# Kernel tuning notes

Hardware: AMD Instinct MI355X
Metric: run time of the kernel (lower is better)

Reference implementation:

```python
import jax, jax.numpy as jnp
import numpy as np

T_MAX = 20  # max_seq_length


def setup_inputs() -> dict:
    key = jax.random.key(0)
    ks = jax.random.split(key, 24)
    B, H, A, V, Tc = 64, 512, 512, 50257, 19
    s = 0.02
    inp = {}
    inp["features"] = jax.random.normal(ks[0], (B, H), jnp.float32)
    inp["captions"] = jax.random.randint(ks[1], (B, Tc), 0, V)
    lens = jax.random.randint(ks[2], (B, 1), 1, T_MAX + 1)
    inp["lengths"] = -jnp.sort(-lens, axis=0)  # descending so sort_ind is identity
    inp["embed_table"] = jax.random.uniform(ks[3], (V, H), jnp.float32, -0.1, 0.1)
    # LSTM cell (PyTorch layout): input = [emb; attended] -> 2H
    inp["W_ih"] = jax.random.normal(ks[4], (4 * H, 2 * H), jnp.float32) * s
    inp["W_hh"] = jax.random.normal(ks[5], (4 * H, H), jnp.float32) * s
    inp["b_ih"] = jnp.zeros((4 * H,), jnp.float32)
    inp["b_hh"] = jnp.zeros((4 * H,), jnp.float32)
    # attention
    inp["W_enc"] = jax.random.normal(ks[6], (H, A), jnp.float32) * s
    inp["b_enc"] = jnp.zeros((A,), jnp.float32)
    inp["W_dec"] = jax.random.normal(ks[7], (H, A), jnp.float32) * s
    inp["b_dec"] = jnp.zeros((A,), jnp.float32)
    inp["W_full"] = jax.random.normal(ks[8], (A, 1), jnp.float32) * s
    inp["b_full"] = jnp.zeros((1,), jnp.float32)
    # init_h / init_c / f_beta / fc
    inp["W_hinit"] = jax.random.normal(ks[9], (H, H), jnp.float32) * s
    inp["b_hinit"] = jnp.zeros((H,), jnp.float32)
    inp["W_cinit"] = jax.random.normal(ks[10], (H, H), jnp.float32) * s
    inp["b_cinit"] = jnp.zeros((H,), jnp.float32)
    inp["W_beta"] = jax.random.normal(ks[11], (H, H), jnp.float32) * s
    inp["b_beta"] = jnp.zeros((H,), jnp.float32)
    inp["W_fc"] = jax.random.uniform(ks[12], (H, V), jnp.float32, -0.1, 0.1)
    inp["b_fc"] = jnp.zeros((V,), jnp.float32)
    return inp


def _decode(features, embed_table, W_ih, W_hh, b_ih, b_hh, W_enc, b_enc,
            W_dec, b_dec, W_full, b_full, W_hinit, b_hinit, W_cinit, b_cinit,
            W_beta, b_beta, W_fc, b_fc, captions, lengths):
    B, H = features.shape
    emb = embed_table[captions]                               # (B, T-1, H)
    embeddings = jnp.concatenate([features[:, None, :], emb], axis=1)  # (B, T, H)
    encoder_out = features[:, None, :]                        # (B, 1, H) num_pixels=1
    mean_enc = encoder_out.mean(axis=1)
    h0 = mean_enc @ W_hinit + b_hinit
    c0 = mean_enc @ W_cinit + b_cinit
    att1 = encoder_out @ W_enc + b_enc                        # (B, 1, A), time-invariant
    lens = lengths[:, 0]

    def step(carry, xs):
        h, c = carry
        emb_t, t = xs
        # attention
        att2 = h @ W_dec + b_dec                              # (B, A)
        e = jax.nn.relu(att1 + att2[:, None, :]) @ W_full + b_full  # (B, 1, 1)
        alpha = jax.nn.softmax(e[..., 0], axis=1)             # (B, 1)
        awe = (encoder_out * alpha[..., None]).sum(axis=1)    # (B, H)
        gate = jax.nn.sigmoid(h @ W_beta + b_beta)
        awe = gate * awe
        # LSTM cell (PyTorch gate order i, f, g, o)
        x = jnp.concatenate([emb_t, awe], axis=1)             # (B, 2H)
        gates = x @ W_ih.T + b_ih + h @ W_hh.T + b_hh
        i, f, g, o = jnp.split(gates, 4, axis=1)
        c_new = jax.nn.sigmoid(f) * c + jax.nn.sigmoid(i) * jnp.tanh(g)
        h_new = jax.nn.sigmoid(o) * jnp.tanh(c_new)
        preds = h_new @ W_fc + b_fc                           # (B, V)
        mask = (t < lens)[:, None]
        h = jnp.where(mask, h_new, h)
        c = jnp.where(mask, c_new, c)
        out_t = jnp.where(mask, preds, jnp.zeros_like(preds))
        return (h, c), out_t

    xs = (embeddings.transpose(1, 0, 2), jnp.arange(T_MAX))
    _, outs = jax.lax.scan(step, (h0, c0), xs)                # (T, B, V)
    return outs.transpose(1, 0, 2)                            # (B, T, V)


def reference(features, captions, lengths, embed_table, W_ih, W_hh, b_ih, b_hh,
              W_enc, b_enc, W_dec, b_dec, W_full, b_full, W_hinit, b_hinit,
              W_cinit, b_cinit, W_beta, b_beta, W_fc, b_fc):
    return _decode(features, embed_table, W_ih, W_hh, b_ih, b_hh, W_enc, b_enc,
                   W_dec, b_dec, W_full, b_full, W_hinit, b_hinit, W_cinit,
                   b_cinit, W_beta, b_beta, W_fc, b_fc, captions, lengths)
```

## Files before the change

### kernel.cpp

```cpp
#include <hip/hip_runtime.h>
#include <hip/hip_bf16.h>


#define VV 50257
#define VP 50304
#define TT 20
#define NWRK 32
#define NTILES 6288

typedef __attribute__((ext_vector_type(4))) float f32x4;
typedef __attribute__((ext_vector_type(8))) short bf16x8;

#define MFMA(a,b,c) __builtin_amdgcn_mfma_f32_16x16x32_bf16((a),(b),(c),0,0,0)

__device__ __forceinline__ unsigned short f2bf(float f){
  union { float f; unsigned int u; } v; v.f = f;
  unsigned int u = v.u;
  return (unsigned short)((u + 0x7FFFu + ((u >> 16) & 1u)) >> 16);
}
__device__ __forceinline__ float sigf(float x){ return 1.f/(1.f + expf(-x)); }

__device__ __forceinline__ void gload_lds16(const unsigned short* g, unsigned short* l){
  __builtin_amdgcn_global_load_lds(
      (const __attribute__((address_space(1))) unsigned int*)g,
      (__attribute__((address_space(3))) unsigned int*)l, 16, 0, 0);
}

__device__ __forceinline__ void co_load16(bf16x8* d, const unsigned short* p){
  asm volatile("global_load_dwordx4 %0, %1, off sc0 sc1" : "=v"(*d) : "v"(p));
}
__device__ __forceinline__ void co_store2(unsigned short* p, unsigned short v){
  asm volatile("global_store_short %0, %1, off sc0 sc1" :: "v"(p), "v"(v) : "memory");
}
__device__ __forceinline__ unsigned int co_load_u32(const unsigned int* p){
  unsigned int r;
  asm volatile("global_load_dword %0, %1, off sc0 sc1\n\ts_waitcnt vmcnt(0)"
               : "=v"(r) : "v"(p) : "memory");
  return r;
}
__device__ __forceinline__ void co_store_u32(unsigned int* p, unsigned int v){
  asm volatile("global_store_dword %0, %1, off sc0 sc1" :: "v"(p), "v"(v) : "memory");
}

__device__ __forceinline__ void gbar(unsigned int* flags, int widx, unsigned target){
  asm volatile("s_waitcnt vmcnt(0)" ::: "memory");
  __syncthreads();
  if(threadIdx.x == 0){
    co_store_u32(flags + widx, target);
  }
  if(threadIdx.x < 64){
    const unsigned int* p = flags + (threadIdx.x & 31);
    for(;;){
      unsigned v = co_load_u32(p);
      if(__all((int)(v >= target))) break;
      __builtin_amdgcn_s_sleep(1);
    }
  }
  __syncthreads();
}

__global__ __launch_bounds__(256) void prep(const float* __restrict__ Wih,
    const float* __restrict__ Whh, unsigned short* __restrict__ Wcomb,
    unsigned short* __restrict__ We,
    const float* __restrict__ Wbeta, unsigned short* __restrict__ Wbt,
    const float* __restrict__ feat, const float* __restrict__ emb,
    const int* __restrict__ cap, unsigned short* __restrict__ EmbMat,
    const float* __restrict__ Whi, const float* __restrict__ bhi,
    const float* __restrict__ Wci, const float* __restrict__ bci,
    unsigned short* __restrict__ xbuf, float* __restrict__ cbuf){
  __shared__ float tile[64][65];
  const int blk = blockIdx.x, tid = threadIdx.x;
  if(blk < 2048){
    int j = blk;
    for(int q=0;q<4;q++){ int k = tid + 256*q;
      float v = (k < 512) ? Whh[j*512 + k] : Wih[j*1024 + k];
      Wcomb[(size_t)j*1024 + k] = f2bf(v); }
    for(int q=0;q<2;q++){ int k = tid + 256*q;
      We[(size_t)j*512 + k] = f2bf(Wih[j*1024 + k]); }
  } else if(blk < 2112){
    int tb = blk - 2048;
    int c0 = (tb & 7)*64, r0 = (tb >> 3)*64;
    int tx = tid & 63, ty = tid >> 6;
    for(int i=0;i<16;i++){
      int r = ty + i*4;
      tile[r][tx] = Wbeta[(size_t)(r0+r)*512 + c0 + tx];
    }
    __syncthreads();
    for(int i=0;i<16;i++){
      int cl = ty + i*4;
      Wbt[(size_t)(c0+cl)*512 + r0 + tx] = f2bf(tile[tx][cl]);
    }
  } else if(blk < 3392){
    int m = blk - 2112; int t = m >> 6, b = m & 63;
    const float* src = (t == 0) ? (feat + b*512) : (emb + (size_t)cap[b*19 + (t-1)]*512);
    for(int q=0;q<2;q++){ int k = tid + 256*q;
      EmbMat[(size_t)m*512 + k] = f2bf(src[k]); }
  } else {
    int b = blk - 3392;
    float ah0 = bhi[tid], ah1 = bhi[tid+256];
    float ac0 = bci[tid], ac1 = bci[tid+256];
    for(int k=0;k<512;k++){
      float f = feat[b*512 + k];
      ah0 += f * Whi[k*512 + tid];     ah1 += f * Whi[k*512 + tid + 256];
      ac0 += f * Wci[k*512 + tid];     ac1 += f * Wci[k*512 + tid + 256];
    }
    xbuf[b*512 + tid] = f2bf(ah0);  xbuf[b*512 + tid + 256] = f2bf(ah1);
    cbuf[b*512 + tid] = ac0;        cbuf[b*512 + tid + 256] = ac1;
  }
}

__global__ __launch_bounds__(256) void gemmE(const unsigned short* __restrict__ Abf,
    const unsigned short* __restrict__ Bbf, const float* __restrict__ bias1,
    const float* __restrict__ bias2, float* __restrict__ Cout, int MT){
  __shared__ __align__(16) unsigned short As[128*64];
  __shared__ __align__(16) unsigned short Bs[128*64];
  const int nwg = gridDim.x;
  const int id = blockIdx.x;
  const int q = nwg >> 3, rr = nwg & 7;
  const int xcd = id & 7, pos = id >> 3;
  const int work = (xcd < rr) ? (xcd*(q+1) + pos) : (rr*(q+1) + (xcd-rr)*q + pos);
  const int m0 = (work % MT) * 128;
  const int n0 = (work / MT) * 128;
  const int tid = threadIdx.x, lane = tid & 63, w = tid >> 6;
  const int wr = w >> 1, wc = w & 1;
  const int lrow = lane >> 3, lcol = (lane & 7) * 8;
  const int l15 = lane & 15, lhi = lane >> 4;

  f32x4 acc[4][4];
#pragma unroll
  for(int i=0;i<4;i++)
#pragma unroll
    for(int j=0;j<4;j++) acc[i][j] = f32x4{0.f,0.f,0.f,0.f};

  for(int k0=0;k0<512;k0+=64){
    __syncthreads();
#pragma unroll
    for(int i=0;i<4;i++){
      int c = w*4 + i;
      int row = c*8 + lrow;
      gload_lds16(Abf + (size_t)(m0+row)*512 + k0 + lcol, As + c*512);
      gload_lds16(Bbf + (size_t)(n0+row)*512 + k0 + lcol, Bs + c*512);
    }
    asm volatile("s_waitcnt vmcnt(0)" ::: "memory");
    __syncthreads();
#pragma unroll
    for(int kk=0;kk<64;kk+=32){
      bf16x8 af[4], bfv[4];
#pragma unroll
      for(int mf=0;mf<4;mf++)
        af[mf] = *(const bf16x8*)(As + (wr*64 + mf*16 + l15)*64 + kk + lhi*8);
#pragma unroll
      for(int nf=0;nf<4;nf++)
        bfv[nf] = *(const bf16x8*)(Bs + (wc*64 + nf*16 + l15)*64 + kk + lhi*8);
#pragma unroll
      for(int mf=0;mf<4;mf++)
#pragma unroll
        for(int nf=0;nf<4;nf++)
          acc[mf][nf] = MFMA(af[mf], bfv[nf], acc[mf][nf]);
    }
  }
#pragma unroll
  for(int mf=0;mf<4;mf++)
#pragma unroll
    for(int nf=0;nf<4;nf++){
      int n = n0 + wc*64 + nf*16 + l15;
#pragma unroll
      for(int r=0;r<4;r++){
        int m = m0 + wr*64 + mf*16 + lhi*4 + r;
        int gate = n >> 9, col = n & 511;
        Cout[((size_t)m*512 + col)*4 + gate] = acc[mf][nf][r] + bias1[n] + bias2[n];
      }
    }
}

__global__ __launch_bounds__(256) void recur(
    const unsigned short* __restrict__ Wcomb,
    const unsigned short* __restrict__ Wbt,
    const float* __restrict__ bbeta,
    const float* __restrict__ feat,
    const float* __restrict__ E4,
    const float* __restrict__ c0,
    const int* __restrict__ lens,
    unsigned short* xbuf,
    unsigned short* awbuf,
    unsigned short* __restrict__ hs,
    unsigned int* ctrs,
    const float* __restrict__ Wfc, unsigned short* __restrict__ Wfct){
  extern __shared__ char LDS[];
  char* WCb = LDS;
  char* WBb = LDS + 131072;
  int* lsh = (int*)LDS;
  const int tid = threadIdx.x;

  if(tid == 0){
    unsigned xcc = 99;
    asm volatile("s_getreg_b32 %0, hwreg(HW_REG_XCC_ID)" : "=s"(xcc));
    unsigned my = 0xffffffffu;
    if(xcc == 0) my = atomicAdd(&ctrs[0], 1u);
    lsh[0] = (my < NWRK) ? 1 : 0;
    lsh[1] = (int)my;
  }
  __syncthreads();
  const int iswork = lsh[0];
  const int widx = lsh[1];
  __syncthreads();

  if(!iswork){
    float (*tile)[65] = (float(*)[65])LDS;
    int tx = tid & 63, ty = tid >> 6;
    for(;;){
      __syncthreads();
      if(tid == 0) lsh[0] = (int)atomicAdd(&ctrs[16], 1u);
      __syncthreads();
      int tb = lsh[0];
      __syncthreads();
      if(tb >= NTILES) return;
      int c0t = (tb % 786)*64, r0 = (tb / 786)*64;
      for(int i=0;i<16;i++){
        int r = ty + i*4; int sc = c0t + tx;
        tile[r][tx] = (sc < VV) ? Wfc[(size_t)(r0+r)*VV + sc] : 0.f;
      }
      __syncthreads();
      for(int i=0;i<16;i++){
        int cl = ty + i*4;
        Wfct[(size_t)(c0t+cl)*512 + r0 + tx] = f2bf(tile[tx][cl]);
      }
    }
  }

  const int lane = tid & 63, w = tid >> 6;
  const int l15 = lane & 15, lhi = lane >> 4;
  const int jj0 = widx * 16;
  const int jj = jj0 + l15;
  const int arow = w*16 + l15;
  unsigned int* flags = &ctrs[32];

  for(int cid = tid; cid < 8192; cid += 256){
    int gr = cid >> 7, cc = cid & 127;
    size_t g = (size_t)(gr >> 4)*512 + jj0 + (gr & 15);
    bf16x8 v = *(const bf16x8*)(Wcomb + g*1024 + cc*8);
    *(bf16x8*)(WCb + gr*2048 + ((cc*16) ^ ((gr & 7) << 4))) = v;
  }
  for(int cid = tid; cid < 1024; cid += 256){
    int r = cid >> 6, cc = cid & 63;
    bf16x8 v = *(const bf16x8*)(Wbt + (size_t)(jj0 + r)*512 + cc*8);
    *(bf16x8*)(WBb + r*1024 + ((cc*16) ^ ((r & 7) << 4))) = v;
  }

  float c_reg[4], fe[4]; int ln[4]; unsigned short hold[4];
#pragma unroll
  for(int r=0;r<4;r++){
    int b = w*16 + lhi*4 + r;
    c_reg[r] = c0[b*512 + jj];
    fe[r]    = feat[b*512 + jj];
    ln[r]    = lens[b];
    hold[r]  = xbuf[b*512 + jj];
  }
  const float bb = bbeta[jj];
  const unsigned short* pAx = xbuf  + (size_t)arow*512 + lhi*8;
  const unsigned short* pAw = awbuf + (size_t)arow*512 + lhi*8;
  __syncthreads();

  for(int t=0;t<TT;t++){
    f32x4 e4v[4];
#pragma unroll
    for(int r=0;r<4;r++){
      int b = w*16 + lhi*4 + r;
      e4v[r] = *(const f32x4*)(E4 + (((size_t)(t*64 + b))*512 + jj)*4);
    }
    bf16x8 a[16];
#pragma unroll
    for(int i=0;i<16;i++) co_load16(&a[i], pAx + i*32);
    asm volatile("s_waitcnt vmcnt(0)" ::: "memory");
    __builtin_amdgcn_sched_barrier(0);

    f32x4 acca = f32x4{0.f,0.f,0.f,0.f};
    f32x4 accg[4];
#pragma unroll
    for(int i=0;i<4;i++) accg[i] = f32x4{0.f,0.f,0.f,0.f};
#pragma unroll
    for(int i=0;i<16;i++){
      int kb2 = i*64 + lhi*16;
      bf16x8 wb = *(const bf16x8*)(WBb + l15*1024 + (kb2 ^ ((l15 & 7) << 4)));
      acca = MFMA(a[i], wb, acca);
#pragma unroll
      for(int nf=0; nf<4; nf++){
        int gr = nf*16 + l15;
        bf16x8 wg = *(const bf16x8*)(WCb + gr*2048 + (kb2 ^ ((gr & 7) << 4)));
        accg[nf] = MFMA(a[i], wg, accg[nf]);
      }
    }
#pragma unroll
    for(int r=0;r<4;r++){
      int b = w*16 + lhi*4 + r;
      float g = sigf(acca[r] + bb);
      co_store2(awbuf + b*512 + jj, f2bf(g * fe[r]));
    }
    gbar(flags, widx, (unsigned)(2*t+1));

#pragma unroll
    for(int i=0;i<16;i++) co_load16(&a[i], pAw + i*32);
    asm volatile("s_waitcnt vmcnt(0)" ::: "memory");
    __builtin_amdgcn_sched_barrier(0);
#pragma unroll
    for(int i=0;i<16;i++){
      int kb2 = 1024 + i*64 + lhi*16;
#pragma unroll
      for(int nf=0; nf<4; nf++){
        int gr = nf*16 + l15;
        bf16x8 wg = *(const bf16x8*)(WCb + gr*2048 + (kb2 ^ ((gr & 7) << 4)));
        accg[nf] = MFMA(a[i], wg, accg[nf]);
      }
    }

#pragma unroll
    for(int r=0;r<4;r++){
      int b = w*16 + lhi*4 + r;
      float iv = sigf(accg[0][r] + e4v[r][0]);
      float fv = sigf(accg[1][r] + e4v[r][1]);
      float gv = tanhf(accg[2][r] + e4v[r][2]);
      float ov = sigf(accg[3][r] + e4v[r][3]);
      float cn = fv*c_reg[r] + iv*gv;
      float hn = ov * tanhf(cn);
      bool valid = t < ln[r];
      if(valid) c_reg[r] = cn;
      unsigned short hb = valid ? f2bf(hn) : hold[r];
      hold[r] = hb;
      hs[((size_t)(t*64 + b))*512 + jj] = hb;
      co_store2(xbuf + b*512 + jj, hb);
    }
    if(t < TT-1) gbar(flags, widx, (unsigned)(2*t+2));
  }
}

__global__ __launch_bounds__(256) void outgemm(
    const unsigned short* __restrict__ hs,
    const unsigned short* __restrict__ Wfct,
    const float* __restrict__ bfc, const int* __restrict__ lens,
    float* __restrict__ out){
  extern __shared__ char LDS[];
  unsigned short* Bs = (unsigned short*)LDS;
  float* et = (float*)(LDS + 131072);
  const int tid = threadIdx.x, lane = tid & 63, w = tid >> 6;
  const int l15 = lane & 15, lhi = lane >> 4;
  const int n0 = blockIdx.x * 128;

#pragma unroll
  for(int i=0;i<32;i++){
    int cid = tid + 256*i;
    int row = cid >> 6, cc = cid & 63;
    bf16x8 v = *(const bf16x8*)(Wfct + (size_t)(n0 + row)*512 + cc*8);
    *(bf16x8*)((char*)Bs + row*1024 + ((cc*16) ^ ((row & 7) << 4))) = v;
  }
  float bias[8]; int lnv[4];
#pragma unroll
  for(int nf=0;nf<8;nf++){
    int n = n0 + nf*16 + l15;
    bias[nf] = (n < VV) ? bfc[n] : 0.f;
  }
#pragma unroll
  for(int r=0;r<4;r++) lnv[r] = lens[w*16 + lhi*4 + r];
  __syncthreads();
  const bool edge = (n0 + 128 > VV);

  for(int t=0;t<TT;t++){
    bf16x8 af[16];
    const unsigned short* pA = hs + (size_t)(t*64 + w*16 + l15)*512 + lhi*8;
#pragma unroll
    for(int i=0;i<16;i++) af[i] = *(const bf16x8*)(pA + i*32);
    f32x4 acc[8];
#pragma unroll
    for(int nf=0;nf<8;nf++) acc[nf] = f32x4{0.f,0.f,0.f,0.f};
#pragma unroll
    for(int i=0;i<16;i++){
      int kb2 = i*64 + lhi*16;
#pragma unroll
      for(int nf=0;nf<8;nf++){
        int gr = nf*16 + l15;
        bf16x8 bv = *(const bf16x8*)((char*)Bs + gr*1024 + (kb2 ^ ((gr & 7) << 4)));
        acc[nf] = MFMA(af[i], bv, acc[nf]);
      }
    }
    for(int h=0; h<2; h++){
      __syncthreads();
      if((w >> 1) == h){
#pragma unroll
        for(int nf=0;nf<8;nf++){
#pragma unroll
          for(int r=0;r<4;r++){
            bool valid = t < lnv[r];
            float v = valid ? (acc[nf][r] + bias[nf]) : 0.f;
            et[((w & 1)*16 + lhi*4 + r)*128 + nf*16 + l15] = v;
          }
        }
      }
      __syncthreads();
#pragma unroll
      for(int qq=0;qq<4;qq++){
        int idx = tid + 256*qq;
        int rowl = idx >> 5, c4 = idx & 31;
        int b = h*32 + rowl;
        const float* er = et + rowl*128;
        size_t bdw = (size_t)(b*20 + t)*VV + n0;
        if(!edge){
          int al = (int)((4 - (bdw & 3)) & 3);
          int chunks = (128 - al) >> 2;
          int tail = (128 - al) & 3;
          if(c4 < chunks){
            int s0 = al + c4*4;
            f32x4 v; v[0]=er[s0]; v[1]=er[s0+1]; v[2]=er[s0+2]; v[3]=er[s0+3];
            *(f32x4*)(out + bdw + s0) = v;
          }
          if(c4 < al) out[bdw + c4] = er[c4];
          if(c4 < tail){ int s1 = al + chunks*4 + c4; out[bdw + s1] = er[s1]; }
        } else {
#pragma unroll
          for(int i2=0;i2<4;i2++){
            int cg = n0 + c4*4 + i2;
            if(cg < VV) out[bdw + (c4*4 + i2)] = er[c4*4 + i2];
          }
        }
      }
    }
  }
}

extern "C" void kernel_launch(void* const* d_in, const int* in_sizes, int n_in,
                              void* d_out, int out_size, void* d_ws, size_t ws_size,
                              hipStream_t stream){
  const float* feat  = (const float*)d_in[0];
  const int*   cap   = (const int*)  d_in[1];
  const int*   lens  = (const int*)  d_in[2];
  const float* emb   = (const float*)d_in[3];
  const float* Wih   = (const float*)d_in[4];
  const float* Whh   = (const float*)d_in[5];
  const float* bih   = (const float*)d_in[6];
  const float* bhh   = (const float*)d_in[7];
  const float* Whi   = (const float*)d_in[14];
  const float* bhi   = (const float*)d_in[15];
  const float* Wci   = (const float*)d_in[16];
  const float* bci   = (const float*)d_in[17];
  const float* Wbeta = (const float*)d_in[18];
  const float* bbeta = (const float*)d_in[19];
  const float* Wfc   = (const float*)d_in[20];
  const float* bfc   = (const float*)d_in[21];
  float* out = (float*)d_out;

  char* ws = (char*)d_ws;
  size_t off = 0;
  auto alloc = [&](size_t bytes)->void*{
    void* p = ws + off; off += (bytes + 1023) & ~(size_t)1023; return p; };
  unsigned short* Wcomb  = (unsigned short*)alloc((size_t)2048*1024*2);
  unsigned short* We     = (unsigned short*)alloc((size_t)2048*512*2);
  unsigned short* Wbt    = (unsigned short*)alloc((size_t)512*512*2);
  unsigned short* Wfct   = (unsigned short*)alloc((size_t)VP*512*2);
  unsigned short* EmbMat = (unsigned short*)alloc((size_t)1280*512*2);
  float*          E4     = (float*)alloc((size_t)1280*2048*4);
  unsigned short* xbuf   = (unsigned short*)alloc((size_t)64*512*2);
  unsigned short* awbuf  = (unsigned short*)alloc((size_t)64*512*2);
  float*          cbuf   = (float*)alloc((size_t)64*512*4);
  unsigned short* hs     = (unsigned short*)alloc((size_t)1280*512*2);
  unsigned int*   ctrs   = (unsigned int*)alloc(256);

  static_cast<void>(hipFuncSetAttribute((const void*)recur,
      hipFuncAttributeMaxDynamicSharedMemorySize, 147456));
  static_cast<void>(hipFuncSetAttribute((const void*)outgemm,
      hipFuncAttributeMaxDynamicSharedMemorySize, 147456));

  hipMemsetAsync(ctrs, 0, 256, stream);

  prep<<<3456, 256, 0, stream>>>(Wih, Whh, Wcomb, We, Wbeta, Wbt, feat, emb,
                                 cap, EmbMat, Whi, bhi, Wci, bci, xbuf, cbuf);

  gemmE<<<160, 256, 0, stream>>>(EmbMat, We, bih, bhh, E4, 10);

  recur<<<2080, 256, 147456, stream>>>(Wcomb, Wbt, bbeta, feat, E4, cbuf, lens,
                                       xbuf, awbuf, hs, ctrs, Wfc, Wfct);

  outgemm<<<393, 256, 147456, stream>>>(hs, Wfct, bfc, lens, out);
}
```

Baseline: 649.4 us.

## Move Wfc transpose to separate kernel, busy-spin idle recur blocks, halve outgemm tile

The Wfc transpose to bf16 no longer runs on the non-worker blocks of the recurrent kernel and gets its own launch. The recurrent grid shrinks to 256 blocks. Non-worker blocks now spin on dummy FMAs until the workers set a completion flag, apparently to keep other XCDs clocked up or busy. The output GEMM uses 64-column tiles with half the LDS, doubling the block count for better occupancy. The transpose no longer overlaps the serial recurrence, and the spinning burns power and CU time.

```diff
diff --git a/kernel.cpp b/kernel.cpp
--- a/kernel.cpp
+++ b/kernel.cpp
@@ -6,7 +6,6 @@
 #define VP 50304
 #define TT 20
 #define NWRK 32
-#define NTILES 6288
 
 typedef __attribute__((ext_vector_type(4))) float f32x4;
 typedef __attribute__((ext_vector_type(8))) short bf16x8;
@@ -109,6 +108,22 @@
   }
 }
 
+__global__ __launch_bounds__(256) void tpose(const float* __restrict__ src,
+    unsigned short* __restrict__ dst){
+  __shared__ float tile[64][65];
+  int c0 = blockIdx.x*64, r0 = blockIdx.y*64;
+  int tx = threadIdx.x & 63, ty = threadIdx.x >> 6;
+  for(int i=0;i<16;i++){
+    int r = ty + i*4; int sc = c0 + tx;
+    tile[r][tx] = (sc < VV) ? src[(size_t)(r0+r)*VV + sc] : 0.f;
+  }
+  __syncthreads();
+  for(int i=0;i<16;i++){
+    int cl = ty + i*4;
+    dst[(size_t)(c0+cl)*512 + r0 + tx] = f2bf(tile[tx][cl]);
+  }
+}
+
 __global__ __launch_bounds__(256) void gemmE(const unsigned short* __restrict__ Abf,
     const unsigned short* __restrict__ Bbf, const float* __restrict__ bias1,
     const float* __restrict__ bias2, float* __restrict__ Cout, int MT){
@@ -184,8 +199,7 @@
     unsigned short* xbuf,
     unsigned short* awbuf,
     unsigned short* __restrict__ hs,
-    unsigned int* ctrs,
-    const float* __restrict__ Wfc, unsigned short* __restrict__ Wfct){
+    unsigned int* ctrs){
   extern __shared__ char LDS[];
   char* WCb = LDS;
   char* WBb = LDS + 131072;
@@ -206,26 +220,16 @@
   __syncthreads();
 
   if(!iswork){
-    float (*tile)[65] = (float(*)[65])LDS;
-    int tx = tid & 63, ty = tid >> 6;
-    for(;;){
-      __syncthreads();
-      if(tid == 0) lsh[0] = (int)atomicAdd(&ctrs[16], 1u);
-      __syncthreads();
-      int tb = lsh[0];
-      __syncthreads();
-      if(tb >= NTILES) return;
-      int c0t = (tb % 786)*64, r0 = (tb / 786)*64;
-      for(int i=0;i<16;i++){
-        int r = ty + i*4; int sc = c0t + tx;
-        tile[r][tx] = (sc < VV) ? Wfc[(size_t)(r0+r)*VV + sc] : 0.f;
-      }
-      __syncthreads();
-      for(int i=0;i<16;i++){
-        int cl = ty + i*4;
-        Wfct[(size_t)(c0t+cl)*512 + r0 + tx] = f2bf(tile[tx][cl]);
-      }
-    }
+    float x = 1.0f + (float)tid;
+    for(int it=0; it<6000; ++it){
+#pragma unroll
+      for(int u=0; u<64; ++u) x = __builtin_fmaf(x, 1.0000001f, 1e-7f);
+      if((it & 63) == 0){
+        if(co_load_u32(&ctrs[3]) != 0) break;
+      }
+    }
+    asm volatile("" :: "v"(x));
+    return;
   }
 
   const int lane = tid & 63, w = tid >> 6;
@@ -331,6 +335,7 @@
     }
     if(t < TT-1) gbar(flags, widx, (unsigned)(2*t+2));
   }
+  if(tid == 0 && widx == 0) co_store_u32(&ctrs[3], 1u);
 }
 
 __global__ __launch_bounds__(256) void outgemm(
@@ -340,42 +345,42 @@
     float* __restrict__ out){
   extern __shared__ char LDS[];
   unsigned short* Bs = (unsigned short*)LDS;
-  float* et = (float*)(LDS + 131072);
+  float* et = (float*)(LDS + 65536);
   const int tid = threadIdx.x, lane = tid & 63, w = tid >> 6;
   const int l15 = lane & 15, lhi = lane >> 4;
-  const int n0 = blockIdx.x * 128;
-
-#pragma unroll
-  for(int i=0;i<32;i++){
+  const int n0 = blockIdx.x * 64;
+
+#pragma unroll
+  for(int i=0;i<16;i++){
     int cid = tid + 256*i;
     int row = cid >> 6, cc = cid & 63;
     bf16x8 v = *(const bf16x8*)(Wfct + (size_t)(n0 + row)*512 + cc*8);
     *(bf16x8*)((char*)Bs + row*1024 + ((cc*16) ^ ((row & 7) << 4))) = v;
   }
-  float bias[8]; int lnv[4];
-#pragma unroll
-  for(int nf=0;nf<8;nf++){
+  float bias[4]; int lnv[4];
+#pragma unroll
+  for(int nf=0;nf<4;nf++){
     int n = n0 + nf*16 + l15;
     bias[nf] = (n < VV) ? bfc[n] : 0.f;
   }
 #pragma unroll
   for(int r=0;r<4;r++) lnv[r] = lens[w*16 + lhi*4 + r];
   __syncthreads();
-  const bool edge = (n0 + 128 > VV);
+  const bool edge = (n0 + 64 > VV);
 
   for(int t=0;t<TT;t++){
     bf16x8 af[16];
     const unsigned short* pA = hs + (size_t)(t*64 + w*16 + l15)*512 + lhi*8;
 #pragma unroll
     for(int i=0;i<16;i++) af[i] = *(const bf16x8*)(pA + i*32);
-    f32x4 acc[8];
-#pragma unroll
-    for(int nf=0;nf<8;nf++) acc[nf] = f32x4{0.f,0.f,0.f,0.f};
+    f32x4 acc[4];
+#pragma unroll
+    for(int nf=0;nf<4;nf++) acc[nf] = f32x4{0.f,0.f,0.f,0.f};
 #pragma unroll
     for(int i=0;i<16;i++){
       int kb2 = i*64 + lhi*16;
 #pragma unroll
-      for(int nf=0;nf<8;nf++){
+      for(int nf=0;nf<4;nf++){
         int gr = nf*16 + l15;
         bf16x8 bv = *(const bf16x8*)((char*)Bs + gr*1024 + (kb2 ^ ((gr & 7) << 4)));
         acc[nf] = MFMA(af[i], bv, acc[nf]);
@@ -385,27 +390,27 @@
       __syncthreads();
       if((w >> 1) == h){
 #pragma unroll
-        for(int nf=0;nf<8;nf++){
+        for(int nf=0;nf<4;nf++){
 #pragma unroll
           for(int r=0;r<4;r++){
             bool valid = t < lnv[r];
             float v = valid ? (acc[nf][r] + bias[nf]) : 0.f;
-            et[((w & 1)*16 + lhi*4 + r)*128 + nf*16 + l15] = v;
+            et[((w & 1)*16 + lhi*4 + r)*64 + nf*16 + l15] = v;
           }
         }
       }
       __syncthreads();
 #pragma unroll
-      for(int qq=0;qq<4;qq++){
+      for(int qq=0;qq<2;qq++){
         int idx = tid + 256*qq;
-        int rowl = idx >> 5, c4 = idx & 31;
+        int rowl = idx >> 4, c4 = idx & 15;
         int b = h*32 + rowl;
-        const float* er = et + rowl*128;
+        const float* er = et + rowl*64;
         size_t bdw = (size_t)(b*20 + t)*VV + n0;
         if(!edge){
           int al = (int)((4 - (bdw & 3)) & 3);
-          int chunks = (128 - al) >> 2;
-          int tail = (128 - al) & 3;
+          int chunks = (64 - al) >> 2;
+          int tail = (64 - al) & 3;
           if(c4 < chunks){
             int s0 = al + c4*4;
             f32x4 v; v[0]=er[s0]; v[1]=er[s0+1]; v[2]=er[s0+2]; v[3]=er[s0+3];
@@ -465,17 +470,19 @@
   static_cast<void>(hipFuncSetAttribute((const void*)recur,
       hipFuncAttributeMaxDynamicSharedMemorySize, 147456));
   static_cast<void>(hipFuncSetAttribute((const void*)outgemm,
-      hipFuncAttributeMaxDynamicSharedMemorySize, 147456));
+      hipFuncAttributeMaxDynamicSharedMemorySize, 73728));
 
   hipMemsetAsync(ctrs, 0, 256, stream);
 
   prep<<<3456, 256, 0, stream>>>(Wih, Whh, Wcomb, We, Wbeta, Wbt, feat, emb,
                                  cap, EmbMat, Whi, bhi, Wci, bci, xbuf, cbuf);
 
+  tpose<<<dim3(786,8), 256, 0, stream>>>(Wfc, Wfct);
+
   gemmE<<<160, 256, 0, stream>>>(EmbMat, We, bih, bhh, E4, 10);
 
-  recur<<<2080, 256, 147456, stream>>>(Wcomb, Wbt, bbeta, feat, E4, cbuf, lens,
-                                       xbuf, awbuf, hs, ctrs, Wfc, Wfct);
-
-  outgemm<<<393, 256, 147456, stream>>>(hs, Wfct, bfc, lens, out);
-}
+  recur<<<256, 256, 147456, stream>>>(Wcomb, Wbt, bbeta, feat, E4, cbuf, lens,
+                                      xbuf, awbuf, hs, ctrs);
+
+  outgemm<<<786, 256, 73728, stream>>>(hs, Wfct, bfc, lens, out);
+}
```

Result: no change. 648.2 us (-0.2%).
